# Kernel tuning notes

Measured on AMD Instinct MI355X. Metric: run time of the kernel, lower is better.

## Reference

```python
import jax, jax.numpy as jnp
from jax import lax
import numpy as np

# Model dims (from MambaVisionEncoder defaults + HF MambaConfig defaults)
HIDDEN = 128      # hidden_dim
DEPTH = 4         # num_hidden_layers
INTER = 4 * HIDDEN  # intermediate_size = 512
STATE = 16        # state_size
DT_RANK = 8       # ceil(hidden/16)
KCONV = 4         # conv_kernel
EPS = 1e-5        # layer_norm_epsilon
B_, T_ = 2, 256
C_, H_, W_ = 3, 224, 224
INPUT_DIM = C_ * H_ * W_


def setup_inputs() -> dict:
    key = jax.random.key(0)
    ks = jax.random.split(key, 8)
    s = 0.02
    return {
        "x": jax.random.normal(ks[0], (B_, T_, C_, H_, W_), jnp.float32),
        # torch Linear weights are [out, in]
        "project_w": jax.random.normal(ks[1], (HIDDEN, INPUT_DIM), jnp.float32) * s,
        "project_b": jnp.zeros((HIDDEN,), jnp.float32),
        "in_proj_w": jax.random.normal(ks[2], (DEPTH, 2 * INTER, HIDDEN), jnp.float32) * s,
        "conv_w": jax.random.normal(ks[3], (DEPTH, INTER, KCONV), jnp.float32) * s,
        "conv_b": jnp.zeros((DEPTH, INTER), jnp.float32),
        "x_proj_w": jax.random.normal(ks[4], (DEPTH, DT_RANK + 2 * STATE, INTER), jnp.float32) * s,
        "dt_proj_w": jax.random.normal(ks[5], (DEPTH, INTER, DT_RANK), jnp.float32) * s,
        "dt_proj_b": jnp.zeros((DEPTH, INTER), jnp.float32),
        # S4D-style init: A_log = log(1..N), broadcast over channels
        "A_log": jnp.log(jnp.broadcast_to(jnp.arange(1, STATE + 1, dtype=jnp.float32), (DEPTH, INTER, STATE))),
        "D_ssm": jnp.ones((DEPTH, INTER), jnp.float32),
        "out_proj_w": jax.random.normal(ks[6], (DEPTH, HIDDEN, INTER), jnp.float32) * s,
        "norm_w": jnp.ones((DEPTH, HIDDEN), jnp.float32),
        "norm_f_w": jnp.ones((HIDDEN,), jnp.float32),
    }


def rmsnorm(x, w):
    var = jnp.mean(jnp.square(x), axis=-1, keepdims=True)
    return x * lax.rsqrt(var + EPS) * w


def mamba_mixer(h, ipw, cw, cb, xpw, dtw, dtb, A_log, Dp, opw):
    # h: [B, T, D]
    Bsz, T, _ = h.shape
    proj = jnp.einsum('btd,ed->bte', h, ipw)          # [B, T, 2I]
    hs, gate = jnp.split(proj, 2, axis=-1)
    hs = hs.transpose(0, 2, 1)                         # [B, I, T]
    # causal depthwise conv1d, kernel KCONV
    conv = lax.conv_general_dilated(
        hs, cw[:, None, :], (1,), [(KCONV - 1, 0)],
        dimension_numbers=('NCH', 'OIH', 'NCH'), feature_group_count=INTER)
    hs = jax.nn.silu(conv + cb[None, :, None])         # [B, I, T]
    ssm_in = jnp.einsum('bit,ei->bte', hs, xpw)        # [B, T, dt_rank+2N]
    dt, Bm, Cm = jnp.split(ssm_in, [DT_RANK, DT_RANK + STATE], axis=-1)
    dt = jax.nn.softplus(jnp.einsum('btr,ir->bti', dt, dtw) + dtb)  # [B, T, I]
    A = -jnp.exp(A_log)                                # [I, N]
    u = hs.transpose(0, 2, 1)                          # [B, T, I]
    dA = jnp.exp(dt[..., None] * A[None, None])        # [B, T, I, N]
    dBu = dt[..., None] * Bm[:, :, None, :] * u[..., None]  # [B, T, I, N]

    def step(state, inp):                              # state: [B, I, N]
        dA_t, dBu_t, C_t = inp
        state = dA_t * state + dBu_t
        y_t = jnp.einsum('bin,bn->bi', state, C_t)
        return state, y_t

    init = jnp.zeros((Bsz, INTER, STATE), hs.dtype)
    _, ys = lax.scan(step, init, (dA.transpose(1, 0, 2, 3), dBu.transpose(1, 0, 2, 3), Cm.transpose(1, 0, 2)))
    y = ys.transpose(1, 0, 2)                          # [B, T, I]
    y = (y + u * Dp[None, None, :]) * jax.nn.silu(gate)
    return jnp.einsum('bti,di->btd', y, opw)           # [B, T, D]


def reference(x, project_w, project_b, in_proj_w, conv_w, conv_b, x_proj_w,
              dt_proj_w, dt_proj_b, A_log, D_ssm, out_proj_w, norm_w, norm_f_w):
    B, T = x.shape[0], x.shape[1]
    flat = x.reshape(B, T, -1)                         # [B, T, input_dim]
    h = jnp.einsum('bti,di->btd', flat, project_w) + project_b  # [B, T, HIDDEN]
    for l in range(DEPTH):
        h = h + mamba_mixer(rmsnorm(h, norm_w[l]), in_proj_w[l], conv_w[l], conv_b[l],
                            x_proj_w[l], dt_proj_w[l], dt_proj_b[l], A_log[l],
                            D_ssm[l], out_proj_w[l])
    return rmsnorm(h, norm_f_w)
```

## Files before the change

kernel.cpp:

```cpp
#include <hip/hip_runtime.h>
#include <hip/hip_bf16.h>

#define HIDDEN 128
#define DEPTH 4
#define INTER 512
#define NSTATE 16
#define DT_RANK 8
#define EPS_RMS 1e-5f
#define MTOK 512
#define KIN 150528

typedef __attribute__((ext_vector_type(8))) short bf16x8;
typedef __attribute__((ext_vector_type(4))) float f32x4;

__device__ __forceinline__ unsigned short f2bf(float f) {
  unsigned int u = __builtin_bit_cast(unsigned int, f);
  u += 0x7fffu + ((u >> 16) & 1u);
  return (unsigned short)(u >> 16);
}
__device__ __forceinline__ float silu_f(float x) {
  return x / (1.0f + __expf(-x));
}

__global__ __launch_bounds__(512) void proj_gemm(
    const float* __restrict__ x, const float* __restrict__ w,
    float* __restrict__ partial)
{
  const int bid = blockIdx.x;
  const int nslab = 18 + (bid < 96 ? 1 : 0);
  const int s0 = bid * 18 + (bid < 96 ? bid : 96);
  __shared__ unsigned short xs[512 * 32];
  __shared__ unsigned short wsm[128 * 32];
  const int tid = threadIdx.x;
  const int lane = tid & 63;
  const int wv = tid >> 6;
  const int fr = lane & 15;
  const int kg = (lane >> 4) * 8;
  const int r8 = tid >> 3;
  const int c4 = (tid & 7) * 4;

  f32x4 acc[4][8];
  #pragma unroll
  for (int mi = 0; mi < 4; ++mi)
    #pragma unroll
    for (int ni = 0; ni < 8; ++ni)
      acc[mi][ni] = (f32x4){0.f, 0.f, 0.f, 0.f};

  float4 rx[8], rw[2];
  {
    const float* xk = x + (size_t)s0 * 32 + c4;
    const float* wk = w + (size_t)s0 * 32 + c4;
    #pragma unroll
    for (int p = 0; p < 8; ++p) rx[p] = *(const float4*)(xk + (size_t)(r8 + p * 64) * KIN);
    #pragma unroll
    for (int p = 0; p < 2; ++p) rw[p] = *(const float4*)(wk + (size_t)(r8 + p * 64) * KIN);
  }

  for (int ks = 0; ks < nslab; ++ks) {
    #pragma unroll
    for (int p = 0; p < 8; ++p) {
      ushort4 bx = {f2bf(rx[p].x), f2bf(rx[p].y), f2bf(rx[p].z), f2bf(rx[p].w)};
      *(ushort4*)&xs[(r8 + p * 64) * 32 + c4] = bx;
    }
    #pragma unroll
    for (int p = 0; p < 2; ++p) {
      ushort4 bw = {f2bf(rw[p].x), f2bf(rw[p].y), f2bf(rw[p].z), f2bf(rw[p].w)};
      *(ushort4*)&wsm[(r8 + p * 64) * 32 + c4] = bw;
    }
    __syncthreads();
    if (ks < nslab - 1) {
      const float* xk = x + (size_t)(s0 + ks + 1) * 32 + c4;
      const float* wk = w + (size_t)(s0 + ks + 1) * 32 + c4;
      #pragma unroll
      for (int p = 0; p < 8; ++p) rx[p] = *(const float4*)(xk + (size_t)(r8 + p * 64) * KIN);
      #pragma unroll
      for (int p = 0; p < 2; ++p) rw[p] = *(const float4*)(wk + (size_t)(r8 + p * 64) * KIN);
    }
    bf16x8 a[4];
    #pragma unroll
    for (int mi = 0; mi < 4; ++mi)
      a[mi] = *(const bf16x8*)&xs[(wv * 64 + mi * 16 + fr) * 32 + kg];
    #pragma unroll
    for (int ni = 0; ni < 8; ++ni) {
      const bf16x8 bfr = *(const bf16x8*)&wsm[(ni * 16 + fr) * 32 + kg];
      #pragma unroll
      for (int mi = 0; mi < 4; ++mi)
        acc[mi][ni] = __builtin_amdgcn_mfma_f32_16x16x32_bf16(a[mi], bfr, acc[mi][ni], 0, 0, 0);
    }
    __syncthreads();
  }
  float* hp = partial + (size_t)(bid & 7) * (MTOK * HIDDEN);
  #pragma unroll
  for (int mi = 0; mi < 4; ++mi)
    #pragma unroll
    for (int ni = 0; ni < 8; ++ni)
      #pragma unroll
      for (int r = 0; r < 4; ++r) {
        const int grow = wv * 64 + mi * 16 + (lane >> 4) * 4 + r;
        const int gcol = ni * 16 + fr;
        atomicAdd(hp + (size_t)grow * HIDDEN + gcol, acc[mi][ni][r]);
      }
}

__global__ __launch_bounds__(512) void fusedA(
    int mode,
    const float* __restrict__ part, const float* __restrict__ pb,
    const float* __restrict__ y_g, const float* __restrict__ gate_g,
    float* __restrict__ h_g,
    const float* __restrict__ opw,
    const float* __restrict__ nw,
    const float* __restrict__ ipw,
    float* __restrict__ hs_g, float* __restrict__ gate_out,
    float* __restrict__ dout)
{
  const int m0 = blockIdx.x * 2;
  const int tid = threadIdx.x;
  const int o2 = tid >> 1;
  const int half = tid & 1;
  const int t = o2 >> 7, d = o2 & 127;
  __shared__ float y2[2][512];
  __shared__ float hrow[2][128];
  __shared__ float hn[2][128];

  float hv;
  if (mode == 0) {
    hv = pb[d];
    #pragma unroll
    for (int s = 0; s < 8; ++s)
      hv += part[(size_t)s * (MTOK * HIDDEN) + (size_t)(m0 + t) * 128 + d];
  } else {
    #pragma unroll
    for (int j = 0; j < 2; ++j) {
      const int o = tid + j * 512;
      const int tt = o >> 9, i = o & 511;
      const float yv = y_g[(size_t)(m0 + tt) * 512 + i];
      const float g  = gate_g[(size_t)(m0 + tt) * 512 + i];
      y2[tt][i] = yv * silu_f(g);
    }
    __syncthreads();
    const float4* yp = (const float4*)(&y2[t][0] + half * 256);
    const float4* wp = (const float4*)(opw + (size_t)d * 512 + half * 256);
    float a0 = 0.f, a1 = 0.f, a2 = 0.f, a3 = 0.f;
    #pragma unroll 8
    for (int kk = 0; kk < 64; ++kk) {
      const float4 yv = yp[kk], wv4 = wp[kk];
      a0 += yv.x * wv4.x; a1 += yv.y * wv4.y;
      a2 += yv.z * wv4.z; a3 += yv.w * wv4.w;
    }
    float a = (a0 + a1) + (a2 + a3);
    a += __shfl_xor(a, 1);
    hv = h_g[(size_t)(m0 + t) * 128 + d] + a;
  }
  if (mode != 2 && half == 0) h_g[(size_t)(m0 + t) * 128 + d] = hv;
  if (half == 0) hrow[t][d] = hv;
  __syncthreads();
  {
    const int wvi = tid >> 6, ln = tid & 63;
    const int tt = wvi & 1;
    const float v0 = hrow[tt][ln], v1 = hrow[tt][ln + 64];
    float ss = v0 * v0 + v1 * v1;
    #pragma unroll
    for (int off = 1; off < 64; off <<= 1) ss += __shfl_xor(ss, off);
    const float rr = rsqrtf(ss * (1.0f / 128.0f) + EPS_RMS);
    if (mode == 2) {
      if (wvi < 2) {
        dout[(size_t)(m0 + tt) * 128 + ln]      = v0 * rr * nw[ln];
        dout[(size_t)(m0 + tt) * 128 + ln + 64] = v1 * rr * nw[ln + 64];
      }
      return;
    }
    if (wvi < 2) {
      hn[tt][ln]      = v0 * rr * nw[ln];
      hn[tt][ln + 64] = v1 * rr * nw[ln + 64];
    }
  }
  __syncthreads();
  #pragma unroll
  for (int j = 0; j < 4; ++j) {
    const int o = tid + j * 512;
    const int tt = o >> 10, e = o & 1023;
    const float4* hp4 = (const float4*)&hn[tt][0];
    const float4* wp4 = (const float4*)(ipw + (size_t)e * 128);
    float a0 = 0.f, a1 = 0.f, a2 = 0.f, a3 = 0.f;
    #pragma unroll
    for (int kk = 0; kk < 32; ++kk) {
      const float4 hvv = hp4[kk], wv4 = wp4[kk];
      a0 += hvv.x * wv4.x; a1 += hvv.y * wv4.y;
      a2 += hvv.z * wv4.z; a3 += hvv.w * wv4.w;
    }
    const float a = (a0 + a1) + (a2 + a3);
    if (e < 512) hs_g[(size_t)(m0 + tt) * 512 + e] = a;
    else         gate_out[(size_t)(m0 + tt) * 512 + (e - 512)] = a;
  }
}

__global__ __launch_bounds__(512) void convxp(
    const float* __restrict__ hs_g, const float* __restrict__ cw,
    const float* __restrict__ cb, const float* __restrict__ xpw,
    const float* __restrict__ dtw, const float* __restrict__ dtb,
    float* __restrict__ uT, float* __restrict__ dtT,
    float* __restrict__ Bm, float* __restrict__ Cm)
{
  const int m0 = blockIdx.x * 2;
  const int b = m0 >> 8, tb0 = m0 & 255;
  const int tid = threadIdx.x;
  __shared__ float hs5[5][512];
  __shared__ float u4[2][512];
  __shared__ float si[2][40];
  for (int o = tid; o < 2560; o += 512) {
    const int j = o >> 9, i = o & 511;
    const int ct = tb0 - 3 + j;
    hs5[j][i] = (ct >= 0) ? hs_g[((size_t)b * 256 + ct) * 512 + i] : 0.f;
  }
  __syncthreads();
  #pragma unroll
  for (int j = 0; j < 2; ++j) {
    const int o = tid + j * 512;
    const int t = o >> 9, i = o & 511;
    const float4 c4v = *(const float4*)(cw + (size_t)i * 4);
    const float s = cb[i] + c4v.x * hs5[t][i] + c4v.y * hs5[t + 1][i]
                          + c4v.z * hs5[t + 2][i] + c4v.w * hs5[t + 3][i];
    const float uu = silu_f(s);
    u4[t][i] = uu;
    uT[((size_t)b * 512 + i) * 256 + tb0 + t] = uu;
  }
  __syncthreads();
  if (tid < 160) {
    const int pid = tid >> 1, half = tid & 1;
    const int t = pid / 40, e = pid % 40;
    const float4* up = (const float4*)(&u4[t][0] + half * 256);
    const float4* wp = (const float4*)(xpw + (size_t)e * 512 + half * 256);
    float a0 = 0.f, a1 = 0.f, a2 = 0.f, a3 = 0.f;
    #pragma unroll 8
    for (int kk = 0; kk < 64; ++kk) {
      const float4 uv = up[kk], wv4 = wp[kk];
      a0 += uv.x * wv4.x; a1 += uv.y * wv4.y;
      a2 += uv.z * wv4.z; a3 += uv.w * wv4.w;
    }
    float a = (a0 + a1) + (a2 + a3);
    a += __shfl_xor(a, 1);
    if (half == 0) si[t][e] = a;
  }
  __syncthreads();
  if (tid < 64) {
    const int t = tid >> 5, q = tid & 31;
    if (q < 16) Bm[(size_t)(m0 + t) * 16 + q] = si[t][8 + q];
    else        Cm[(size_t)(m0 + t) * 16 + (q - 16)] = si[t][24 + (q - 16)];
  }
  #pragma unroll
  for (int j = 0; j < 2; ++j) {
    const int o = tid + j * 512;
    const int i = o >> 1, t = o & 1;
    float a0 = dtb[i];
    const float* dr = dtw + (size_t)i * 8;
    #pragma unroll
    for (int r = 0; r < 8; ++r) a0 += si[t][r] * dr[r];
    const float sp = (a0 > 20.f) ? a0 : log1pf(__expf(a0));
    dtT[((size_t)b * 512 + i) * 256 + tb0 + t] = sp;
  }
}

__global__ __launch_bounds__(256) void scan_k(
    const float* __restrict__ uT, const float* __restrict__ dtT,
    const float* __restrict__ Bm, const float* __restrict__ Cm,
    const float* __restrict__ Alog, const float* __restrict__ Dssm,
    float* __restrict__ y_g)
{
  const int blk = blockIdx.x;
  const int b = blk >> 9, i = blk & 511;
  const int tid = threadIdx.x;
  __shared__ float dt_r[256], u_r[256];
  __shared__ float B_l[256][17], C_l[256][17];
  __shared__ float e_l[16][17], P_l[16][17];
  dt_r[tid] = dtT[((size_t)b * 512 + i) * 256 + tid];
  u_r[tid]  = uT[((size_t)b * 512 + i) * 256 + tid];
  #pragma unroll
  for (int j = 0; j < 16; ++j) {
    const int o = tid + j * 256;
    B_l[o >> 4][o & 15] = Bm[(size_t)b * 4096 + o];
    C_l[o >> 4][o & 15] = Cm[(size_t)b * 4096 + o];
  }
  __syncthreads();
  const int c = tid >> 4, n = tid & 15;
  const float Av = -__expf(Alog[(size_t)i * 16 + n]);
  const float Dv = Dssm[i];
  float aj[16], xj[16];
  float s = 0.f, P = 1.f;
  #pragma unroll
  for (int j = 0; j < 16; ++j) {
    const int t = c * 16 + j;
    const float dtv = dt_r[t];
    const float a = __expf(Av * dtv);
    const float xx = dtv * B_l[t][n] * u_r[t];
    aj[j] = a; xj[j] = xx;
    s = a * s + xx; P *= a;
  }
  e_l[c][n] = s; P_l[c][n] = P;
  __syncthreads();
  float s0 = 0.f;
  for (int cc = 0; cc < c; ++cc)
    s0 = P_l[cc][n] * s0 + e_l[cc][n];
  s = s0;
  #pragma unroll
  for (int j = 0; j < 16; ++j) {
    const int t = c * 16 + j;
    s = aj[j] * s + xj[j];
    float p = s * C_l[t][n];
    p += __shfl_xor(p, 1); p += __shfl_xor(p, 2);
    p += __shfl_xor(p, 4); p += __shfl_xor(p, 8);
    if (n == 0)
      y_g[((size_t)b * 256 + t) * 512 + i] = p + u_r[t] * Dv;
  }
}

extern "C" void kernel_launch(void* const* d_in, const int* in_sizes, int n_in,
                              void* d_out, int out_size, void* d_ws, size_t ws_size,
                              hipStream_t stream)
{
  (void)in_sizes; (void)n_in; (void)out_size; (void)ws_size;
  const float* x    = (const float*)d_in[0];
  const float* pw   = (const float*)d_in[1];
  const float* pb   = (const float*)d_in[2];
  const float* ipw  = (const float*)d_in[3];
  const float* cw   = (const float*)d_in[4];
  const float* cb   = (const float*)d_in[5];
  const float* xpw  = (const float*)d_in[6];
  const float* dtw  = (const float*)d_in[7];
  const float* dtb  = (const float*)d_in[8];
  const float* Alog = (const float*)d_in[9];
  const float* Dssm = (const float*)d_in[10];
  const float* opw  = (const float*)d_in[11];
  const float* nw   = (const float*)d_in[12];
  const float* nwf  = (const float*)d_in[13];
  float* out = (float*)d_out;

  float* ws   = (float*)d_ws;
  float* part = ws;
  float* h    = part + 8 * 65536;
  float* hs   = h + 65536;
  float* gate = hs + 262144;
  float* uT   = gate + 262144;
  float* dtT  = uT + 262144;
  float* Bm   = dtT + 262144;
  float* Cm   = Bm + 8192;
  float* y    = Cm + 8192;

  hipMemsetAsync(part, 0, 8 * 65536 * sizeof(float), stream);
  proj_gemm<<<dim3(256), 512, 0, stream>>>(x, pw, part);

  fusedA<<<dim3(256), 512, 0, stream>>>(0, part, pb, nullptr, nullptr, h,
                                        nullptr, nw, ipw, hs, gate, nullptr);
  for (int l = 0; l < DEPTH; ++l) {
    convxp<<<dim3(256), 512, 0, stream>>>(
        hs, cw + (size_t)l * 2048, cb + (size_t)l * 512,
        xpw + (size_t)l * 40 * 512, dtw + (size_t)l * 512 * 8,
        dtb + (size_t)l * 512, uT, dtT, Bm, Cm);
    scan_k<<<dim3(1024), 256, 0, stream>>>(
        uT, dtT, Bm, Cm, Alog + (size_t)l * 512 * 16, Dssm + (size_t)l * 512, y);
    if (l < DEPTH - 1)
      fusedA<<<dim3(256), 512, 0, stream>>>(1, nullptr, nullptr, y, gate, h,
          opw + (size_t)l * 128 * 512, nw + (size_t)(l + 1) * 128,
          ipw + (size_t)(l + 1) * 1024 * 128, hs, gate, nullptr);
    else
      fusedA<<<dim3(256), 512, 0, stream>>>(2, nullptr, nullptr, y, gate, h,
          opw + (size_t)l * 128 * 512, nwf, nullptr, nullptr, nullptr, out);
  }
}
```

Before: 448.5 us.

## Retile projection GEMM into 64x64 output tiles with split-K partial stores

The big projection GEMM is restructured so each block computes a 64x64 output tile over a contiguous K range of 256-wide chunks, instead of the full 512x128 output over short 32-wide slabs. The LDS is double-buffered with an XOR swizzle, and results go as plain stores into 16 separate partial buffers, which removes the atomics and the memset. Global reads become long contiguous row segments per thread rather than strided 32-element pieces, aiming for better DRAM streaming. In exchange, x and w are re-read across the tile grid (each x row is read by two N tiles), each wave does fewer MFMAs per LDS load, and the reduction kernel must sum 16 partials.

```diff
diff --git a/kernel.cpp b/kernel.cpp
--- a/kernel.cpp
+++ b/kernel.cpp
@@ -27,79 +27,87 @@
     float* __restrict__ partial)
 {
   const int bid = blockIdx.x;
-  const int nslab = 18 + (bid < 96 ? 1 : 0);
-  const int s0 = bid * 18 + (bid < 96 ? bid : 96);
-  __shared__ unsigned short xs[512 * 32];
-  __shared__ unsigned short wsm[128 * 32];
+  const int mb = bid & 7;
+  const int nb = (bid >> 3) & 1;
+  const int kb = bid >> 4;
+  const int nchunk = 36 + (kb < 12 ? 1 : 0);
+  const int cb0 = kb * 36 + (kb < 12 ? kb : 12);
+  __shared__ unsigned short sm[2][32768];
+
   const int tid = threadIdx.x;
   const int lane = tid & 63;
   const int wv = tid >> 6;
+  const int wm = wv >> 1;
+  const int wn = wv & 1;
   const int fr = lane & 15;
-  const int kg = (lane >> 4) * 8;
-  const int r8 = tid >> 3;
-  const int c4 = (tid & 7) * 4;
-
-  f32x4 acc[4][8];
-  #pragma unroll
-  for (int mi = 0; mi < 4; ++mi)
-    #pragma unroll
-    for (int ni = 0; ni < 8; ++ni)
-      acc[mi][ni] = (f32x4){0.f, 0.f, 0.f, 0.f};
-
-  float4 rx[8], rw[2];
+  const int kq = lane >> 4;
+  const int rL = tid >> 3;
+  const int cL = tid & 7;
+
+  f32x4 acc[2];
+  acc[0] = (f32x4){0.f, 0.f, 0.f, 0.f};
+  acc[1] = (f32x4){0.f, 0.f, 0.f, 0.f};
+
+  const float* xrow = x + (size_t)(mb * 64 + rL) * KIN + cL * 4;
+  const float* wrow = w + (size_t)(nb * 64 + rL) * KIN + cL * 4;
+
+  float4 rx[8], rw[8];
   {
-    const float* xk = x + (size_t)s0 * 32 + c4;
-    const float* wk = w + (size_t)s0 * 32 + c4;
-    #pragma unroll
-    for (int p = 0; p < 8; ++p) rx[p] = *(const float4*)(xk + (size_t)(r8 + p * 64) * KIN);
-    #pragma unroll
-    for (int p = 0; p < 2; ++p) rw[p] = *(const float4*)(wk + (size_t)(r8 + p * 64) * KIN);
-  }
-
-  for (int ks = 0; ks < nslab; ++ks) {
+    const size_t k0 = (size_t)cb0 * 256;
+    #pragma unroll
+    for (int p = 0; p < 8; ++p) rx[p] = *(const float4*)(xrow + k0 + p * 32);
+    #pragma unroll
+    for (int p = 0; p < 8; ++p) rw[p] = *(const float4*)(wrow + k0 + p * 32);
+  }
+
+  for (int cc = 0; cc < nchunk; ++cc) {
+    unsigned short* xs = &sm[cc & 1][0];
+    unsigned short* ws_ = &sm[cc & 1][16384];
+    const int sb = rL * 512 + cL * 8;
+    const int swz = (rL & 7) << 4;
     #pragma unroll
     for (int p = 0; p < 8; ++p) {
       ushort4 bx = {f2bf(rx[p].x), f2bf(rx[p].y), f2bf(rx[p].z), f2bf(rx[p].w)};
-      *(ushort4*)&xs[(r8 + p * 64) * 32 + c4] = bx;
-    }
-    #pragma unroll
-    for (int p = 0; p < 2; ++p) {
+      *(ushort4*)((char*)xs + ((sb + p * 64) ^ swz)) = bx;
+    }
+    #pragma unroll
+    for (int p = 0; p < 8; ++p) {
       ushort4 bw = {f2bf(rw[p].x), f2bf(rw[p].y), f2bf(rw[p].z), f2bf(rw[p].w)};
-      *(ushort4*)&wsm[(r8 + p * 64) * 32 + c4] = bw;
+      *(ushort4*)((char*)ws_ + ((sb + p * 64) ^ swz)) = bw;
     }
     __syncthreads();
-    if (ks < nslab - 1) {
-      const float* xk = x + (size_t)(s0 + ks + 1) * 32 + c4;
-      const float* wk = w + (size_t)(s0 + ks + 1) * 32 + c4;
+    if (cc + 1 < nchunk) {
+      const size_t k0 = (size_t)(cb0 + cc + 1) * 256;
       #pragma unroll
-      for (int p = 0; p < 8; ++p) rx[p] = *(const float4*)(xk + (size_t)(r8 + p * 64) * KIN);
+      for (int p = 0; p < 8; ++p) rx[p] = *(const float4*)(xrow + k0 + p * 32);
       #pragma unroll
-      for (int p = 0; p < 2; ++p) rw[p] = *(const float4*)(wk + (size_t)(r8 + p * 64) * KIN);
-    }
-    bf16x8 a[4];
-    #pragma unroll
-    for (int mi = 0; mi < 4; ++mi)
-      a[mi] = *(const bf16x8*)&xs[(wv * 64 + mi * 16 + fr) * 32 + kg];
-    #pragma unroll
-    for (int ni = 0; ni < 8; ++ni) {
-      const bf16x8 bfr = *(const bf16x8*)&wsm[(ni * 16 + fr) * 32 + kg];
-      #pragma unroll
-      for (int mi = 0; mi < 4; ++mi)
-        acc[mi][ni] = __builtin_amdgcn_mfma_f32_16x16x32_bf16(a[mi], bfr, acc[mi][ni], 0, 0, 0);
+      for (int p = 0; p < 8; ++p) rw[p] = *(const float4*)(wrow + k0 + p * 32);
+    }
+    const unsigned short* xs2 = &sm[cc & 1][0];
+    const unsigned short* ws2 = &sm[cc & 1][16384];
+    const int arow = wm * 16 + fr;
+    const int br0 = wn * 32 + fr;
+    const int aswz = (fr & 7) << 4;
+    #pragma unroll
+    for (int ks = 0; ks < 8; ++ks) {
+      const int kbyte = ks * 64 + kq * 16;
+      const bf16x8 a  = *(const bf16x8*)((const char*)xs2 + ((arow * 512 + kbyte) ^ aswz));
+      const bf16x8 b0 = *(const bf16x8*)((const char*)ws2 + ((br0 * 512 + kbyte) ^ aswz));
+      const bf16x8 b1 = *(const bf16x8*)((const char*)ws2 + (((br0 + 16) * 512 + kbyte) ^ aswz));
+      acc[0] = __builtin_amdgcn_mfma_f32_16x16x32_bf16(a, b0, acc[0], 0, 0, 0);
+      acc[1] = __builtin_amdgcn_mfma_f32_16x16x32_bf16(a, b1, acc[1], 0, 0, 0);
     }
     __syncthreads();
   }
-  float* hp = partial + (size_t)(bid & 7) * (MTOK * HIDDEN);
-  #pragma unroll
-  for (int mi = 0; mi < 4; ++mi)
-    #pragma unroll
-    for (int ni = 0; ni < 8; ++ni)
-      #pragma unroll
-      for (int r = 0; r < 4; ++r) {
-        const int grow = wv * 64 + mi * 16 + (lane >> 4) * 4 + r;
-        const int gcol = ni * 16 + fr;
-        atomicAdd(hp + (size_t)grow * HIDDEN + gcol, acc[mi][ni][r]);
-      }
+  float* hp = partial + (size_t)kb * (MTOK * HIDDEN);
+  #pragma unroll
+  for (int j = 0; j < 2; ++j)
+    #pragma unroll
+    for (int r = 0; r < 4; ++r) {
+      const int row = mb * 64 + wm * 16 + kq * 4 + r;
+      const int col = nb * 64 + wn * 32 + j * 16 + fr;
+      hp[(size_t)row * HIDDEN + col] = acc[j][r];
+    }
 }
 
 __global__ __launch_bounds__(512) void fusedA(
@@ -126,7 +134,7 @@
   if (mode == 0) {
     hv = pb[d];
     #pragma unroll
-    for (int s = 0; s < 8; ++s)
+    for (int s = 0; s < 16; ++s)
       hv += part[(size_t)s * (MTOK * HIDDEN) + (size_t)(m0 + t) * 128 + d];
   } else {
     #pragma unroll
@@ -336,7 +344,7 @@
 
   float* ws   = (float*)d_ws;
   float* part = ws;
-  float* h    = part + 8 * 65536;
+  float* h    = part + 16 * 65536;
   float* hs   = h + 65536;
   float* gate = hs + 262144;
   float* uT   = gate + 262144;
@@ -345,7 +353,6 @@
   float* Cm   = Bm + 8192;
   float* y    = Cm + 8192;
 
-  hipMemsetAsync(part, 0, 8 * 65536 * sizeof(float), stream);
   proj_gemm<<<dim3(256), 512, 0, stream>>>(x, pw, part);
 
   fusedA<<<dim3(256), 512, 0, stream>>>(0, part, pb, nullptr, nullptr, h,
```

New measurement: 454.6 us. Within noise of the previous version (+1.4%).
